# Optimization experiments

Measured on AMD Instinct MI355X. Metric: run time of the kernel, lower is better.

The kernel has to match this reference:

```python
import jax, jax.numpy as jnp
import numpy as np

B, F, V, DW, H, K, T = 32, 2048, 12000, 300, 512, 3, 32
START_ID, END_ID = 1, 2
NEG = -1e9


def lstm(x, h, c, Wx, Wh, b):
    # BasicLSTMCell with forget_bias=1.0
    z = x @ Wx + h @ Wh + b  # [N, 4H]
    i, f, g, o = jnp.split(z, 4, axis=-1)
    c2 = jax.nn.sigmoid(f + 1.0) * c + jax.nn.sigmoid(i) * jnp.tanh(g)
    h2 = jax.nn.sigmoid(o) * jnp.tanh(c2)
    return h2, c2


def beam_decode(E, Wx, Wh, b, Wl, bl, img):
    Bn = img.shape[0]
    img_t = jnp.repeat(img, K, axis=0)  # tile_batch: [B*K, F]
    h = jnp.zeros((Bn * K, H), img.dtype)
    c = jnp.zeros_like(h)
    beam_lp = jnp.tile(jnp.array([0.0] + [NEG] * (K - 1), img.dtype), (Bn, 1))  # [B,K]
    prev = jnp.full((Bn, K), START_ID, jnp.int32)
    finished = jnp.zeros((Bn, K), bool)
    lengths = jnp.zeros((Bn, K), jnp.int32)
    ids = jnp.zeros((Bn, K, T), jnp.int32)
    end_row = jnp.where(jnp.arange(V) == END_ID, 0.0, NEG)  # finished beams only emit END

    def step(carry, t):
        h, c, beam_lp, prev, finished, lengths, ids = carry
        x = jnp.concatenate([E[prev.reshape(-1)], img_t], axis=-1)  # [B*K, DW+F]
        h2, c2 = lstm(x, h, c, Wx, Wh, b)
        lp = jax.nn.log_softmax(h2 @ Wl + bl).reshape(Bn, K, V)
        lp = jnp.where(finished[:, :, None], end_row, lp)
        total = (beam_lp[:, :, None] + lp).reshape(Bn, K * V)
        scores, idx = jax.lax.top_k(total, K)  # [B,K]
        parent = idx // V
        word = (idx % V).astype(jnp.int32)
        g2 = lambda a: jnp.take_along_axis(a, parent, axis=1)
        g3 = lambda a: jnp.take_along_axis(a, parent[:, :, None], axis=1)
        h2 = g3(h2.reshape(Bn, K, H)).reshape(Bn * K, H)
        c2 = g3(c2.reshape(Bn, K, H)).reshape(Bn * K, H)
        ids = g3(ids).at[:, :, t].set(word)  # reorder hypotheses, append word
        fin_p = g2(finished)
        len_p = g2(lengths)
        lengths = jnp.where(fin_p, len_p, len_p + 1)
        finished = fin_p | (word == END_ID)
        return (h2, c2, scores, word, finished, lengths, ids), None

    carry, _ = jax.lax.scan(step, (h, c, beam_lp, prev, finished, lengths, ids), jnp.arange(T))
    return carry[6], carry[5]  # ids [B,K,T], lengths [B,K]


def teacher_rnn(E, Wx, Wh, b, img_t, seq_inputs, lengths):
    # dynamic_rnn semantics: zero outputs and frozen state past sequence_length
    N, L = seq_inputs.shape
    emb = E[seq_inputs]  # [N, L, DW]
    h0 = jnp.zeros((N, H), E.dtype)
    c0 = jnp.zeros_like(h0)

    def step(carry, xs):
        h, c = carry
        x_t, t = xs
        xin = jnp.concatenate([x_t, img_t], axis=-1)
        h2, c2 = lstm(xin, h, c, Wx, Wh, b)
        active = (t < lengths)[:, None]
        h = jnp.where(active, h2, h)
        c = jnp.where(active, c2, c)
        return (h, c), jnp.where(active, h2, 0.0)

    _, outs = jax.lax.scan(step, (h0, c0), (emb.transpose(1, 0, 2), jnp.arange(L)))
    return outs.transpose(1, 0, 2)  # [N, L, H]


def setup_inputs() -> dict:
    key = jax.random.key(0)
    ks = jax.random.split(key, 6)
    return {
        "mean_image_features": jax.random.normal(ks[0], (B, F), jnp.float32),
        "embeddings": jax.random.normal(ks[1], (V, DW), jnp.float32) * 0.1,
        "Wx": jax.random.normal(ks[2], (DW + F, 4 * H), jnp.float32) / np.sqrt(DW + F),
        "Wh": jax.random.normal(ks[3], (H, 4 * H), jnp.float32) / np.sqrt(H),
        "b_lstm": jnp.zeros((4 * H,), jnp.float32),
        "W_logits": jax.random.normal(ks[4], (H, V), jnp.float32) / np.sqrt(H),
        "b_logits": jnp.zeros((V,), jnp.float32),
    }


def reference(mean_image_features, embeddings, Wx, Wh, b_lstm, W_logits, b_logits):
    Bn = mean_image_features.shape[0]
    ids, lengths = beam_decode(embeddings, Wx, Wh, b_lstm, W_logits, b_logits, mean_image_features)
    seq_inputs = jnp.concatenate(
        [jnp.full((Bn, K, 1), START_ID, jnp.int32), ids], axis=2
    ).reshape(Bn * K, T + 1)
    img_t = jnp.repeat(mean_image_features, K, axis=0)
    acts = teacher_rnn(embeddings, Wx, Wh, b_lstm, img_t, seq_inputs, lengths.reshape(-1))
    logits = (acts @ W_logits + b_logits).reshape(Bn, K, T + 1, V)
    return logits, jnp.argmax(logits, axis=-1).astype(jnp.int32)
```

## Files before the change

### kernel.cpp

```cpp
#include <hip/hip_runtime.h>
#include <hip/hip_bf16.h>
#include <math.h>

#define NB   32
#define FDIM 2048
#define VV   12000
#define DWW  300
#define HH   512
#define KW   3
#define TDEC 32
#define SEQ  33
#define NK   96
#define G4   2048
#define START_ID 1
#define END_ID   2
#define NROWS 3168
#define NLB   188
#define INTMX 0x7fffffff
#define FLOORF (-3.0e38f)

typedef float f4v __attribute__((ext_vector_type(4)));
__device__ __forceinline__ void nt_store4(float* p, float4 v){
  f4v t; t.x=v.x; t.y=v.y; t.z=v.z; t.w=v.w;
  __builtin_nontemporal_store(t, (f4v*)p);
}

__device__ __forceinline__ float sigf(float x){ return 1.0f/(1.0f+expf(-x)); }

__device__ __forceinline__ unsigned short f2b(float x){
  __hip_bfloat16 b = __float2bfloat16(x);
  return *reinterpret_cast<unsigned short*>(&b);
}

__device__ __forceinline__ void ins3(float v, int i, float tv[3], int ti[3]){
  if (v > tv[0] || (v == tv[0] && i < ti[0])){
    tv[2]=tv[1]; ti[2]=ti[1]; tv[1]=tv[0]; ti[1]=ti[0]; tv[0]=v; ti[0]=i;
  } else if (v > tv[1] || (v == tv[1] && i < ti[1])){
    tv[2]=tv[1]; ti[2]=ti[1]; tv[1]=v; ti[1]=i;
  } else if (v > tv[2] || (v == tv[2] && i < ti[2])){
    tv[2]=v; ti[2]=i;
  }
}

__device__ __forceinline__ void flag_arrive(int* cnt){
  __hip_atomic_fetch_add(cnt, 1, __ATOMIC_RELEASE, __HIP_MEMORY_SCOPE_AGENT);
}
__device__ __forceinline__ void flag_wait(int* cnt, int target){
  while (__hip_atomic_load(cnt, __ATOMIC_ACQUIRE, __HIP_MEMORY_SCOPE_AGENT) < target)
    __builtin_amdgcn_s_sleep(1);
}

struct SArgs {
  const float *E, *Wx, *Wh, *Wl, *blog;
  float *P, *c2, *h2s, *zp, *partA, *beam_lp, *rowamax;
  int *prev, *finished, *lengths, *parst;
  int *cnt0, *cnt1;
  void *Lst;
};

__global__ __launch_bounds__(128) void k_pimg(const float* __restrict__ img,
                                              const float* __restrict__ Wx,
                                              float* __restrict__ parts)
{
  int colb = blockIdx.x, fb = blockIdx.y, tid = threadIdx.x;
  int col = colb*128 + tid;
  int f0 = fb*128;
  __shared__ float s_img[32][128];
  for (int r=0;r<32;r++) s_img[r][tid] = img[r*FDIM + f0 + tid];
  __syncthreads();
  float acc[32];
  #pragma unroll
  for (int r=0;r<32;r++) acc[r]=0.f;
  for (int f2=0; f2<128; ++f2){
    float w = Wx[(size_t)(DWW + f0 + f2)*G4 + col];
    #pragma unroll
    for (int r=0;r<32;r++) acc[r] += w * s_img[r][f2];
  }
  #pragma unroll
  for (int r=0;r<32;r++) parts[(size_t)fb*(32*G4) + r*G4 + col] = acc[r];
}

__global__ __launch_bounds__(512) void k_prep(const float* __restrict__ parts,
    const float* __restrict__ bls, const float* __restrict__ blog,
    float* __restrict__ P, float* __restrict__ beam_lp, int* __restrict__ prev,
    int* __restrict__ finished, int* __restrict__ lengths, int* __restrict__ cnts,
    float* __restrict__ bamax)
{
  int bid = blockIdx.x, tid = threadIdx.x;
  int gid = bid*512 + tid;
  float s = bls[gid & (G4-1)];
  for (int fb=0; fb<16; ++fb) s += parts[(size_t)fb*(32*G4) + gid];
  P[gid] = s;
  if (bid==0 && tid<NK){
    beam_lp[tid] = (tid%KW==0)?0.f:-1e9f;
    prev[tid]=START_ID; finished[tid]=0; lengths[tid]=0;
  }
  if (bid==1 && tid<2*TDEC) cnts[tid]=0;
  if (bid==2){
    __shared__ float s_rf[8]; __shared__ int s_ri[8];
    float bv=FLOORF; int bi=INTMX;
    for (int i=tid;i<VV;i+=512){
      float v=blog[i];
      if (v>bv || (v==bv && i<bi)){ bv=v; bi=i; }
    }
    #pragma unroll
    for (int d=1;d<64;d<<=1){
      float ov=__shfl_xor(bv,d); int oi=__shfl_xor(bi,d);
      if (ov>bv || (ov==bv && oi<bi)){ bv=ov; bi=oi; }
    }
    if ((tid&63)==0){ s_rf[tid>>6]=bv; s_ri[tid>>6]=bi; }
    __syncthreads();
    if (tid==0){
      for (int w=1;w<8;w++)
        if (s_rf[w]>bv || (s_rf[w]==bv && s_ri[w]<bi)){ bv=s_rf[w]; bi=s_ri[w]; }
      bamax[0] = (float)bi;
    }
  }
}

__global__ __launch_bounds__(512) void k_step1(SArgs a, int t)
{
  int bid = blockIdx.x, tid = threadIdx.x;
  __shared__ float smem[96*17 + 16*64];
  __shared__ int sprev[NK], spar[NK];
  if (t>0 && tid<NK){ sprev[tid]=a.prev[tid]; spar[tid]=a.parst[(t-1)*NK+tid]; }
  __syncthreads();

  {
    int colblk = bid & 31, p = bid >> 5;
    int col0 = colblk*64;
    int ks = p*104, ke = ks+104; if (ke>812) ke=812;
    float* sA = smem;
    float* sB = smem + 96*17;
    int tx = tid&15, ty = tid>>4;
    float4 acc[3];
    #pragma unroll
    for (int r=0;r<3;r++) acc[r]=make_float4(0.f,0.f,0.f,0.f);
    for (int k0=ks;k0<ke;k0+=16){
      int bk = ke-k0; if (bk>16) bk=16;
      for (int i=tid;i<96*16;i+=512){
        int n=i>>4, kk=i&15;
        float v=0.f;
        if (kk<bk){
          int kg=k0+kk;
          if (kg<DWW){
            int w = (t==0)?START_ID:sprev[n];
            v = a.E[(size_t)w*DWW+kg];
          } else if (t>0){
            v = a.h2s[((size_t)(t-1)*NK + spar[n])*HH + (kg-DWW)];
          }
        }
        sA[n*17+kk]=v;
      }
      for (int i=tid;i<16*64;i+=512){
        int kk=i>>6, cc=i&63;
        float v=0.f;
        if (kk<bk){
          int kg=k0+kk;
          v = (kg<DWW) ? a.Wx[(size_t)kg*G4+col0+cc] : a.Wh[(size_t)(kg-DWW)*G4+col0+cc];
        }
        sB[i]=v;
      }
      __syncthreads();
      #pragma unroll
      for (int kk=0;kk<16;++kk){
        float4 b4 = *(const float4*)&sB[kk*64+tx*4];
        #pragma unroll
        for (int rr=0;rr<3;rr++){
          float av = sA[(ty+rr*32)*17+kk];
          acc[rr].x += av*b4.x; acc[rr].y += av*b4.y;
          acc[rr].z += av*b4.z; acc[rr].w += av*b4.w;
        }
      }
      __syncthreads();
    }
    float* zpp = a.zp + (size_t)p*NK*G4;
    #pragma unroll
    for (int rr=0;rr<3;rr++)
      *(float4*)&zpp[(size_t)(ty+rr*32)*G4 + col0 + tx*4] = acc[rr];
  }
  __syncthreads();
  if (tid==0) flag_arrive(&a.cnt0[t]);
  if (bid >= NK) return;

  if (tid==0) flag_wait(&a.cnt0[t], 256);
  __syncthreads();
  {
    int n = bid, m = tid, bb = n/KW;
    const float* Pr = a.P + (size_t)bb*G4;
    float zi=Pr[m], zf=Pr[HH+m], zg=Pr[2*HH+m], zo=Pr[3*HH+m];
    for (int p=0;p<8;p++){
      const float* zz = a.zp + (size_t)p*NK*G4 + (size_t)n*G4;
      zi+=zz[m]; zf+=zz[HH+m]; zg+=zz[2*HH+m]; zo+=zz[3*HH+m];
    }
    float cold = (t==0) ? 0.f : a.c2[(size_t)((t-1)&1)*NK*HH + (size_t)spar[n]*HH + m];
    float c2v = sigf(zf+1.0f)*cold + sigf(zi)*tanhf(zg);
    float h2v = sigf(zo)*tanhf(c2v);
    a.c2[(size_t)(t&1)*NK*HH + (size_t)n*HH + m] = c2v;
    a.h2s[((size_t)t*NK+n)*HH + m] = h2v;
  }
}

template<int BF>
__global__ __launch_bounds__(512) void k_step2(SArgs a, int t)
{
  int bid = blockIdx.x, tid = threadIdx.x;
  __shared__ float smem[96*36 + 32*64];
  __shared__ float s_lse[KW], s_tv3[KW*3];
  __shared__ int   s_ti3[KW*3];

  {
    int col0 = bid*64;
    float* sA = smem;
    float* sB = smem + 96*36;
    int tx=tid&15, ty=tid>>4;
    float4 acc[3];
    #pragma unroll
    for (int r=0;r<3;r++) acc[r]=make_float4(0.f,0.f,0.f,0.f);
    for (int k0=0;k0<HH;k0+=32){
      for (int i=tid;i<768;i+=512){
        int row=i>>3, kq=(i&7)*4;
        *(float4*)&sA[row*36+kq] = *(const float4*)&a.h2s[((size_t)t*NK+row)*HH + k0+kq];
      }
      {
        int kk=tid>>4, c4=(tid&15)*4;
        int col=col0+c4;
        float4 v = make_float4(0.f,0.f,0.f,0.f);
        if (col < VV) v = *(const float4*)&a.Wl[(size_t)(k0+kk)*VV+col];
        *(float4*)&sB[kk*64+c4]=v;
      }
      __syncthreads();
      #pragma unroll
      for (int kk=0;kk<32;++kk){
        float4 b4 = *(const float4*)&sB[kk*64+tx*4];
        #pragma unroll
        for (int rr=0;rr<3;rr++){
          float av = sA[(ty+rr*32)*36+kk];
          acc[rr].x += av*b4.x; acc[rr].y += av*b4.y;
          acc[rr].z += av*b4.z; acc[rr].w += av*b4.w;
        }
      }
      __syncthreads();
    }
    int colg = col0 + tx*4;
    bool cval = colg < VV;
    float4 bias = make_float4(0.f,0.f,0.f,0.f);
    if (cval) bias = *(const float4*)&a.blog[colg];
    #pragma unroll
    for (int rr=0;rr<3;rr++){
      int row = ty + rr*32;
      float v0,v1,v2,v3;
      if (cval){
        v0=acc[rr].x+bias.x; v1=acc[rr].y+bias.y;
        v2=acc[rr].z+bias.z; v3=acc[rr].w+bias.w;
        size_t off = (size_t)(t*NK+row)*VV + colg;
        if (BF){
          ushort4 u;
          u.x=f2b(v0); u.y=f2b(v1); u.z=f2b(v2); u.w=f2b(v3);
          *(ushort4*)((unsigned short*)a.Lst + off) = u;
        } else {
          *(float4*)((float*)a.Lst + off) = make_float4(v0,v1,v2,v3);
        }
      } else { v0=v1=v2=v3=-INFINITY; }
      float m = fmaxf(fmaxf(v0,v1),fmaxf(v2,v3));
      #pragma unroll
      for (int d=1;d<16;d<<=1) m = fmaxf(m,__shfl_xor(m,d));
      float tv[3]={-INFINITY,-INFINITY,-INFINITY};
      int   ti[3]={INTMX,INTMX,INTMX};
      float s=0.f;
      if (cval){
        ins3(v0,colg,tv,ti); ins3(v1,colg+1,tv,ti);
        ins3(v2,colg+2,tv,ti); ins3(v3,colg+3,tv,ti);
        s = expf(v0-m)+expf(v1-m)+expf(v2-m)+expf(v3-m);
      }
      #pragma unroll
      for (int d=1;d<16;d<<=1){
        s += __shfl_xor(s,d);
        float p0=__shfl_xor(tv[0],d),p1=__shfl_xor(tv[1],d),p2=__shfl_xor(tv[2],d);
        int q0=__shfl_xor(ti[0],d),q1=__shfl_xor(ti[1],d),q2=__shfl_xor(ti[2],d);
        ins3(p0,q0,tv,ti); ins3(p1,q1,tv,ti); ins3(p2,q2,tv,ti);
      }
      if (tx==0){
        float* rp = a.partA + ((size_t)row*NLB + bid)*8;
        *(float4*)rp = make_float4(m,s,tv[0],tv[1]);
        *((float4*)rp+1) = make_float4(tv[2],__int_as_float(ti[0]),__int_as_float(ti[1]),__int_as_float(ti[2]));
      }
    }
  }
  __syncthreads();
  if (tid==0) flag_arrive(&a.cnt1[t]);
  if (bid >= NB) return;

  if (tid==0) flag_wait(&a.cnt1[t], NLB);
  __syncthreads();
  {
    int b = bid;
    int wv = tid>>6, lane = tid&63;
    if (wv < KW){
      int n = b*KW+wv;
      float M=FLOORF, S=0.f;
      float tv[3]={FLOORF,FLOORF,FLOORF}; int ti[3]={INTMX,INTMX,INTMX};
      for (int i=lane;i<NLB;i+=64){
        const float* rp = a.partA + ((size_t)n*NLB+i)*8;
        float4 r0=*(const float4*)rp, r1=*((const float4*)rp+1);
        float nm = fmaxf(M,r0.x);
        S = S*expf(M-nm) + r0.y*expf(r0.x-nm);
        M = nm;
        ins3(r0.z,__float_as_int(r1.y),tv,ti);
        ins3(r0.w,__float_as_int(r1.z),tv,ti);
        ins3(r1.x,__float_as_int(r1.w),tv,ti);
      }
      #pragma unroll
      for (int d=1;d<64;d<<=1){
        float Mo=__shfl_xor(M,d), So=__shfl_xor(S,d);
        float nm=fmaxf(M,Mo);
        S = S*expf(M-nm)+So*expf(Mo-nm);
        M=nm;
        float p0=__shfl_xor(tv[0],d),p1=__shfl_xor(tv[1],d),p2=__shfl_xor(tv[2],d);
        int q0=__shfl_xor(ti[0],d),q1=__shfl_xor(ti[1],d),q2=__shfl_xor(ti[2],d);
        ins3(p0,q0,tv,ti); ins3(p1,q1,tv,ti); ins3(p2,q2,tv,ti);
      }
      if (lane==0){
        s_lse[wv] = M + logf(S);
        #pragma unroll
        for (int j=0;j<3;j++){ s_tv3[wv*3+j]=tv[j]; s_ti3[wv*3+j]=ti[j]; }
        a.rowamax[t*NK+n] = (float)ti[0];
      }
    }
    __syncthreads();
    if (tid==0){
      float cv[3]={FLOORF,FLOORF,FLOORF}; int cf[3]={INTMX,INTMX,INTMX};
      for (int k=0;k<KW;k++){
        int n=b*KW+k;
        if (a.finished[n]){
          ins3(a.beam_lp[n], k*VV+END_ID, cv,cf);
        } else {
          float blp=a.beam_lp[n], lse=s_lse[k];
          for (int j=0;j<3;j++)
            ins3(blp + (s_tv3[k*3+j]-lse), k*VV+s_ti3[k*3+j], cv,cf);
        }
      }
      int fin_old[KW], len_old[KW];
      for (int j=0;j<KW;j++){ fin_old[j]=a.finished[b*KW+j]; len_old[j]=a.lengths[b*KW+j]; }
      for (int kp=0;kp<KW;kp++){
        int par=cf[kp]/VV, word=cf[kp]-par*VV;
        a.beam_lp[b*KW+kp]=cv[kp];
        a.prev[b*KW+kp]=word;
        a.parst[t*NK + b*KW+kp] = b*KW+par;
        int fp=fin_old[par];
        a.lengths[b*KW+kp] = fp?len_old[par]:(len_old[par]+1);
        a.finished[b*KW+kp] = fp | (word==END_ID);
      }
    }
  }
}

__global__ __launch_bounds__(128) void k_backtrack(const int* __restrict__ parst,
                                                   const int* __restrict__ lengths,
                                                   int* __restrict__ rowsrc)
{
  int n = threadIdx.x;
  if (n >= NK) return;
  int b = n / KW;
  int len = lengths[n];
  rowsrc[n*SEQ + TDEC] = -1;
  int a = n;
  for (int tau = TDEC-1; tau >= 1; --tau){
    int p = parst[tau*NK + a];
    rowsrc[n*SEQ + tau] = (tau < len) ? (tau*NK + p) : -1;
    a = p;
  }
  rowsrc[n*SEQ + 0] = b*KW;
}

template<int BF>
__global__ __launch_bounds__(512) void k_gather(const void* __restrict__ Lst,
    const int* __restrict__ rowsrc, const float* __restrict__ rowamax,
    const float* __restrict__ bamax, const float* __restrict__ blog,
    float* __restrict__ out)
{
  int row = blockIdx.x, tid = threadIdx.x;
  int src = rowsrc[row];
  float* orow = out + (size_t)row*VV;
  if (src >= 0){
    if (BF){
      const unsigned short* L = (const unsigned short*)Lst + (size_t)src*VV;
      for (int j=tid;j<VV/4;j+=512){
        ushort4 u = *(const ushort4*)&L[j*4];
        float4 v;
        v.x = __uint_as_float(((unsigned)u.x)<<16);
        v.y = __uint_as_float(((unsigned)u.y)<<16);
        v.z = __uint_as_float(((unsigned)u.z)<<16);
        v.w = __uint_as_float(((unsigned)u.w)<<16);
        nt_store4(&orow[j*4], v);
      }
    } else {
      const float* L = (const float*)Lst + (size_t)src*VV;
      for (int j=tid;j<VV/4;j+=512){
        float4 v = *(const float4*)&L[j*4];
        nt_store4(&orow[j*4], v);
      }
    }
    if (tid==0) out[(size_t)NROWS*VV + row] = rowamax[src];
  } else {
    for (int j=tid;j<VV/4;j+=512){
      float4 v = *(const float4*)&blog[j*4];
      nt_store4(&orow[j*4], v);
    }
    if (tid==0) out[(size_t)NROWS*VV + row] = bamax[0];
  }
}

extern "C" void kernel_launch(void* const* d_in, const int* in_sizes, int n_in,
                              void* d_out, int out_size, void* d_ws, size_t ws_size,
                              hipStream_t stream) {
  (void)in_sizes; (void)n_in; (void)out_size;
  const float* img  = (const float*)d_in[0];
  const float* E    = (const float*)d_in[1];
  const float* Wx   = (const float*)d_in[2];
  const float* Wh   = (const float*)d_in[3];
  const float* bls  = (const float*)d_in[4];
  const float* Wl   = (const float*)d_in[5];
  const float* blog = (const float*)d_in[6];
  float* out = (float*)d_out;

  float* ws = (float*)d_ws;
  size_t o = 0;
  float* P       = ws+o; o += (size_t)NB*G4;
  float* c2      = ws+o; o += (size_t)2*NK*HH;
  float* h2s     = ws+o; o += (size_t)TDEC*NK*HH;
  float* zp      = ws+o; o += (size_t)8*NK*G4;
  float* partA   = ws+o; o += (size_t)NK*NLB*8;
  float* beam_lp = ws+o; o += 128;
  float* rowamax = ws+o; o += (size_t)TDEC*NK;
  float* bamax   = ws+o; o += 4;
  int* prev      = (int*)(ws+o); o += 128;
  int* finished  = (int*)(ws+o); o += 128;
  int* lengths   = (int*)(ws+o); o += 128;
  int* parst     = (int*)(ws+o); o += (size_t)TDEC*NK;
  int* rowsrc    = (int*)(ws+o); o += 3328;
  int* cnts      = (int*)(ws+o); o += 64;
  o = (o+3) & ~(size_t)3;
  void* Lst      = (void*)(ws+o);

  bool f32 = (ws_size/4 > o) && ((ws_size/4 - o) >= (size_t)TDEC*NK*VV);

  SArgs a;
  a.E=E; a.Wx=Wx; a.Wh=Wh; a.Wl=Wl; a.blog=blog;
  a.P=P; a.c2=c2; a.h2s=h2s; a.zp=zp; a.partA=partA;
  a.beam_lp=beam_lp; a.rowamax=rowamax;
  a.prev=prev; a.finished=finished; a.lengths=lengths; a.parst=parst;
  a.cnt0=cnts; a.cnt1=cnts+TDEC;
  a.Lst=Lst;

  k_pimg<<<dim3(16,16),128,0,stream>>>(img, Wx, zp);
  k_prep<<<128,512,0,stream>>>(zp, bls, blog, P, beam_lp, prev, finished, lengths, cnts, bamax);

  if (f32){
    for (int t=0;t<TDEC;t++){
      k_step1<<<256,512,0,stream>>>(a,t);
      k_step2<0><<<NLB,512,0,stream>>>(a,t);
    }
    k_backtrack<<<1,128,0,stream>>>(parst, lengths, rowsrc);
    k_gather<0><<<NROWS,512,0,stream>>>(Lst,rowsrc,rowamax,bamax,blog,out);
  } else {
    for (int t=0;t<TDEC;t++){
      k_step1<<<256,512,0,stream>>>(a,t);
      k_step2<1><<<NLB,512,0,stream>>>(a,t);
    }
    k_backtrack<<<1,128,0,stream>>>(parst, lengths, rowsrc);
    k_gather<1><<<NROWS,512,0,stream>>>(Lst,rowsrc,rowamax,bamax,blog,out);
  }
}
```

Before: 3.069 ms.

## Fuse per-step decode kernels into one persistent cooperative kernel with flag barriers

Replaces the 64 per-timestep launches (step1/step2) plus the backtrack kernel with a single cooperatively launched persistent kernel of 256 blocks. The stages within each step are ordered by atomic-counter flag barriers, with an end-of-step barrier over the beam-update blocks. This removes kernel launch gaps and lets blocks run ahead between stages, at the cost of spin-waiting and one grid-wide wait per step. It also switches the fp32 logits stores to nontemporal stores.

```diff
diff --git a/kernel.cpp b/kernel.cpp
--- a/kernel.cpp
+++ b/kernel.cpp
@@ -16,6 +16,8 @@
 #define END_ID   2
 #define NROWS 3168
 #define NLB   188
+#define GRID  256
+#define BLK   512
 #define INTMX 0x7fffffff
 #define FLOORF (-3.0e38f)
 
@@ -42,19 +44,22 @@
   }
 }
 
-__device__ __forceinline__ void flag_arrive(int* cnt){
+__device__ __forceinline__ void bar_arrive(int* cnt){
   __hip_atomic_fetch_add(cnt, 1, __ATOMIC_RELEASE, __HIP_MEMORY_SCOPE_AGENT);
 }
-__device__ __forceinline__ void flag_wait(int* cnt, int target){
-  while (__hip_atomic_load(cnt, __ATOMIC_ACQUIRE, __HIP_MEMORY_SCOPE_AGENT) < target)
-    __builtin_amdgcn_s_sleep(1);
-}
-
-struct SArgs {
+__device__ __forceinline__ void bar_wait(int* cnt, int target){
+  if (threadIdx.x==0){
+    while (__hip_atomic_load(cnt, __ATOMIC_ACQUIRE, __HIP_MEMORY_SCOPE_AGENT) < target)
+      __builtin_amdgcn_s_sleep(1);
+  }
+  __syncthreads();
+}
+
+struct PArgs {
   const float *E, *Wx, *Wh, *Wl, *blog;
   float *P, *c2, *h2s, *zp, *partA, *beam_lp, *rowamax;
-  int *prev, *finished, *lengths, *parst;
-  int *cnt0, *cnt1;
+  int *prev, *finished, *lengths, *parst, *rowsrc;
+  int *fZ, *fG, *fL, *fS;
   void *Lst;
 };
 
@@ -95,7 +100,7 @@
     beam_lp[tid] = (tid%KW==0)?0.f:-1e9f;
     prev[tid]=START_ID; finished[tid]=0; lengths[tid]=0;
   }
-  if (bid==1 && tid<2*TDEC) cnts[tid]=0;
+  if (bid==1 && tid<4*TDEC) cnts[tid]=0;
   if (bid==2){
     __shared__ float s_rf[8]; __shared__ int s_ri[8];
     float bv=FLOORF; int bi=INTMX;
@@ -118,259 +123,253 @@
   }
 }
 
-__global__ __launch_bounds__(512) void k_step1(SArgs a, int t)
-{
-  int bid = blockIdx.x, tid = threadIdx.x;
-  __shared__ float smem[96*17 + 16*64];
-  __shared__ int sprev[NK], spar[NK];
-  if (t>0 && tid<NK){ sprev[tid]=a.prev[tid]; spar[tid]=a.parst[(t-1)*NK+tid]; }
-  __syncthreads();
-
-  {
-    int colblk = bid & 31, p = bid >> 5;
-    int col0 = colblk*64;
-    int ks = p*104, ke = ks+104; if (ke>812) ke=812;
-    float* sA = smem;
-    float* sB = smem + 96*17;
-    int tx = tid&15, ty = tid>>4;
-    float4 acc[3];
-    #pragma unroll
-    for (int r=0;r<3;r++) acc[r]=make_float4(0.f,0.f,0.f,0.f);
-    for (int k0=ks;k0<ke;k0+=16){
-      int bk = ke-k0; if (bk>16) bk=16;
-      for (int i=tid;i<96*16;i+=512){
-        int n=i>>4, kk=i&15;
-        float v=0.f;
-        if (kk<bk){
-          int kg=k0+kk;
-          if (kg<DWW){
-            int w = (t==0)?START_ID:sprev[n];
-            v = a.E[(size_t)w*DWW+kg];
-          } else if (t>0){
-            v = a.h2s[((size_t)(t-1)*NK + spar[n])*HH + (kg-DWW)];
-          }
-        }
-        sA[n*17+kk]=v;
-      }
-      for (int i=tid;i<16*64;i+=512){
-        int kk=i>>6, cc=i&63;
-        float v=0.f;
-        if (kk<bk){
-          int kg=k0+kk;
-          v = (kg<DWW) ? a.Wx[(size_t)kg*G4+col0+cc] : a.Wh[(size_t)(kg-DWW)*G4+col0+cc];
-        }
-        sB[i]=v;
-      }
-      __syncthreads();
-      #pragma unroll
-      for (int kk=0;kk<16;++kk){
-        float4 b4 = *(const float4*)&sB[kk*64+tx*4];
-        #pragma unroll
-        for (int rr=0;rr<3;rr++){
-          float av = sA[(ty+rr*32)*17+kk];
-          acc[rr].x += av*b4.x; acc[rr].y += av*b4.y;
-          acc[rr].z += av*b4.z; acc[rr].w += av*b4.w;
-        }
-      }
-      __syncthreads();
-    }
-    float* zpp = a.zp + (size_t)p*NK*G4;
-    #pragma unroll
-    for (int rr=0;rr<3;rr++)
-      *(float4*)&zpp[(size_t)(ty+rr*32)*G4 + col0 + tx*4] = acc[rr];
-  }
-  __syncthreads();
-  if (tid==0) flag_arrive(&a.cnt0[t]);
-  if (bid >= NK) return;
-
-  if (tid==0) flag_wait(&a.cnt0[t], 256);
-  __syncthreads();
-  {
-    int n = bid, m = tid, bb = n/KW;
-    const float* Pr = a.P + (size_t)bb*G4;
-    float zi=Pr[m], zf=Pr[HH+m], zg=Pr[2*HH+m], zo=Pr[3*HH+m];
-    for (int p=0;p<8;p++){
-      const float* zz = a.zp + (size_t)p*NK*G4 + (size_t)n*G4;
-      zi+=zz[m]; zf+=zz[HH+m]; zg+=zz[2*HH+m]; zo+=zz[3*HH+m];
-    }
-    float cold = (t==0) ? 0.f : a.c2[(size_t)((t-1)&1)*NK*HH + (size_t)spar[n]*HH + m];
-    float c2v = sigf(zf+1.0f)*cold + sigf(zi)*tanhf(zg);
-    float h2v = sigf(zo)*tanhf(c2v);
-    a.c2[(size_t)(t&1)*NK*HH + (size_t)n*HH + m] = c2v;
-    a.h2s[((size_t)t*NK+n)*HH + m] = h2v;
-  }
-}
-
 template<int BF>
-__global__ __launch_bounds__(512) void k_step2(SArgs a, int t)
+__global__ __launch_bounds__(BLK) void k_persist(PArgs a)
 {
   int bid = blockIdx.x, tid = threadIdx.x;
   __shared__ float smem[96*36 + 32*64];
+  __shared__ int sprev[NK], spar[NK];
   __shared__ float s_lse[KW], s_tv3[KW*3];
   __shared__ int   s_ti3[KW*3];
 
-  {
-    int col0 = bid*64;
-    float* sA = smem;
-    float* sB = smem + 96*36;
-    int tx=tid&15, ty=tid>>4;
-    float4 acc[3];
-    #pragma unroll
-    for (int r=0;r<3;r++) acc[r]=make_float4(0.f,0.f,0.f,0.f);
-    for (int k0=0;k0<HH;k0+=32){
-      for (int i=tid;i<768;i+=512){
-        int row=i>>3, kq=(i&7)*4;
-        *(float4*)&sA[row*36+kq] = *(const float4*)&a.h2s[((size_t)t*NK+row)*HH + k0+kq];
-      }
-      {
-        int kk=tid>>4, c4=(tid&15)*4;
-        int col=col0+c4;
-        float4 v = make_float4(0.f,0.f,0.f,0.f);
-        if (col < VV) v = *(const float4*)&a.Wl[(size_t)(k0+kk)*VV+col];
-        *(float4*)&sB[kk*64+c4]=v;
-      }
+  for (int t=0;t<TDEC;++t){
+    if (tid<NK){ sprev[tid]=a.prev[tid]; if (t>0) spar[tid]=a.parst[(t-1)*NK+tid]; }
+    __syncthreads();
+
+    {
+      int colblk = bid & 31, p = bid >> 5;
+      int col0 = colblk*64;
+      int ks = p*104, ke = ks+104; if (ke>812) ke=812;
+      float* sA = smem;
+      float* sB = smem + 96*17;
+      int tx = tid&15, ty = tid>>4;
+      float4 acc[3];
+      #pragma unroll
+      for (int r=0;r<3;r++) acc[r]=make_float4(0.f,0.f,0.f,0.f);
+      for (int k0=ks;k0<ke;k0+=16){
+        int bk = ke-k0; if (bk>16) bk=16;
+        for (int i=tid;i<96*16;i+=BLK){
+          int n=i>>4, kk=i&15;
+          float v=0.f;
+          if (kk<bk){
+            int kg=k0+kk;
+            if (kg<DWW){
+              int w = (t==0)?START_ID:sprev[n];
+              v = a.E[(size_t)w*DWW+kg];
+            } else if (t>0){
+              v = a.h2s[((size_t)(t-1)*NK + spar[n])*HH + (kg-DWW)];
+            }
+          }
+          sA[n*17+kk]=v;
+        }
+        for (int i=tid;i<16*64;i+=BLK){
+          int kk=i>>6, cc=i&63;
+          float v=0.f;
+          if (kk<bk){
+            int kg=k0+kk;
+            v = (kg<DWW) ? a.Wx[(size_t)kg*G4+col0+cc] : a.Wh[(size_t)(kg-DWW)*G4+col0+cc];
+          }
+          sB[i]=v;
+        }
+        __syncthreads();
+        #pragma unroll
+        for (int kk=0;kk<16;++kk){
+          float4 b4 = *(const float4*)&sB[kk*64+tx*4];
+          #pragma unroll
+          for (int rr=0;rr<3;rr++){
+            float av = sA[(ty+rr*32)*17+kk];
+            acc[rr].x += av*b4.x; acc[rr].y += av*b4.y;
+            acc[rr].z += av*b4.z; acc[rr].w += av*b4.w;
+          }
+        }
+        __syncthreads();
+      }
+      float* zpp = a.zp + (size_t)p*NK*G4;
+      #pragma unroll
+      for (int rr=0;rr<3;rr++)
+        *(float4*)&zpp[(size_t)(ty+rr*32)*G4 + col0 + tx*4] = acc[rr];
+    }
+    __syncthreads();
+    if (tid==0) bar_arrive(&a.fZ[t]);
+
+    if (bid < NK){
+      bar_wait(&a.fZ[t], GRID);
+      int n = bid, m = tid, bb = n/KW;
+      const float* Pr = a.P + (size_t)bb*G4;
+      float zi=Pr[m], zf=Pr[HH+m], zg=Pr[2*HH+m], zo=Pr[3*HH+m];
+      for (int p=0;p<8;p++){
+        const float* zz = a.zp + (size_t)p*NK*G4 + (size_t)n*G4;
+        zi+=zz[m]; zf+=zz[HH+m]; zg+=zz[2*HH+m]; zo+=zz[3*HH+m];
+      }
+      float cold = (t==0) ? 0.f : a.c2[(size_t)((t-1)&1)*NK*HH + (size_t)spar[n]*HH + m];
+      float c2v = sigf(zf+1.0f)*cold + sigf(zi)*tanhf(zg);
+      float h2v = sigf(zo)*tanhf(c2v);
+      a.c2[(size_t)(t&1)*NK*HH + (size_t)n*HH + m] = c2v;
+      a.h2s[((size_t)t*NK+n)*HH + m] = h2v;
       __syncthreads();
+      if (tid==0) bar_arrive(&a.fG[t]);
+    }
+
+    if (bid < NLB){
+      bar_wait(&a.fG[t], NK);
+      int col0 = bid*64;
+      float* sA = smem;
+      float* sB = smem + 96*36;
+      int tx=tid&15, ty=tid>>4;
+      float4 acc[3];
       #pragma unroll
-      for (int kk=0;kk<32;++kk){
-        float4 b4 = *(const float4*)&sB[kk*64+tx*4];
+      for (int r=0;r<3;r++) acc[r]=make_float4(0.f,0.f,0.f,0.f);
+      for (int k0=0;k0<HH;k0+=32){
+        for (int i=tid;i<768;i+=BLK){
+          int row=i>>3, kq=(i&7)*4;
+          *(float4*)&sA[row*36+kq] = *(const float4*)&a.h2s[((size_t)t*NK+row)*HH + k0+kq];
+        }
+        {
+          int kk=tid>>4, c4=(tid&15)*4;
+          int col=col0+c4;
+          float4 v = make_float4(0.f,0.f,0.f,0.f);
+          if (col < VV) v = *(const float4*)&a.Wl[(size_t)(k0+kk)*VV+col];
+          *(float4*)&sB[kk*64+c4]=v;
+        }
+        __syncthreads();
         #pragma unroll
-        for (int rr=0;rr<3;rr++){
-          float av = sA[(ty+rr*32)*36+kk];
-          acc[rr].x += av*b4.x; acc[rr].y += av*b4.y;
-          acc[rr].z += av*b4.z; acc[rr].w += av*b4.w;
+        for (int kk=0;kk<32;++kk){
+          float4 b4 = *(const float4*)&sB[kk*64+tx*4];
+          #pragma unroll
+          for (int rr=0;rr<3;rr++){
+            float av = sA[(ty+rr*32)*36+kk];
+            acc[rr].x += av*b4.x; acc[rr].y += av*b4.y;
+            acc[rr].z += av*b4.z; acc[rr].w += av*b4.w;
+          }
+        }
+        __syncthreads();
+      }
+      int colg = col0 + tx*4;
+      bool cval = colg < VV;
+      float4 bias = make_float4(0.f,0.f,0.f,0.f);
+      if (cval) bias = *(const float4*)&a.blog[colg];
+      #pragma unroll
+      for (int rr=0;rr<3;rr++){
+        int row = ty + rr*32;
+        float v0,v1,v2,v3;
+        if (cval){
+          v0=acc[rr].x+bias.x; v1=acc[rr].y+bias.y;
+          v2=acc[rr].z+bias.z; v3=acc[rr].w+bias.w;
+          size_t off = (size_t)(t*NK+row)*VV + colg;
+          if (BF){
+            ushort4 u;
+            u.x=f2b(v0); u.y=f2b(v1); u.z=f2b(v2); u.w=f2b(v3);
+            *(ushort4*)((unsigned short*)a.Lst + off) = u;
+          } else {
+            nt_store4((float*)a.Lst + off, make_float4(v0,v1,v2,v3));
+          }
+        } else { v0=v1=v2=v3=-INFINITY; }
+        float m = fmaxf(fmaxf(v0,v1),fmaxf(v2,v3));
+        #pragma unroll
+        for (int d=1;d<16;d<<=1) m = fmaxf(m,__shfl_xor(m,d));
+        float tv[3]={-INFINITY,-INFINITY,-INFINITY};
+        int   ti[3]={INTMX,INTMX,INTMX};
+        float s=0.f;
+        if (cval){
+          ins3(v0,colg,tv,ti); ins3(v1,colg+1,tv,ti);
+          ins3(v2,colg+2,tv,ti); ins3(v3,colg+3,tv,ti);
+          s = expf(v0-m)+expf(v1-m)+expf(v2-m)+expf(v3-m);
+        }
+        #pragma unroll
+        for (int d=1;d<16;d<<=1){
+          s += __shfl_xor(s,d);
+          float p0=__shfl_xor(tv[0],d),p1=__shfl_xor(tv[1],d),p2=__shfl_xor(tv[2],d);
+          int q0=__shfl_xor(ti[0],d),q1=__shfl_xor(ti[1],d),q2=__shfl_xor(ti[2],d);
+          ins3(p0,q0,tv,ti); ins3(p1,q1,tv,ti); ins3(p2,q2,tv,ti);
+        }
+        if (tx==0){
+          float* rp = a.partA + ((size_t)row*NLB + bid)*8;
+          *(float4*)rp = make_float4(m,s,tv[0],tv[1]);
+          *((float4*)rp+1) = make_float4(tv[2],__int_as_float(ti[0]),__int_as_float(ti[1]),__int_as_float(ti[2]));
         }
       }
       __syncthreads();
-    }
-    int colg = col0 + tx*4;
-    bool cval = colg < VV;
-    float4 bias = make_float4(0.f,0.f,0.f,0.f);
-    if (cval) bias = *(const float4*)&a.blog[colg];
-    #pragma unroll
-    for (int rr=0;rr<3;rr++){
-      int row = ty + rr*32;
-      float v0,v1,v2,v3;
-      if (cval){
-        v0=acc[rr].x+bias.x; v1=acc[rr].y+bias.y;
-        v2=acc[rr].z+bias.z; v3=acc[rr].w+bias.w;
-        size_t off = (size_t)(t*NK+row)*VV + colg;
-        if (BF){
-          ushort4 u;
-          u.x=f2b(v0); u.y=f2b(v1); u.z=f2b(v2); u.w=f2b(v3);
-          *(ushort4*)((unsigned short*)a.Lst + off) = u;
-        } else {
-          *(float4*)((float*)a.Lst + off) = make_float4(v0,v1,v2,v3);
-        }
-      } else { v0=v1=v2=v3=-INFINITY; }
-      float m = fmaxf(fmaxf(v0,v1),fmaxf(v2,v3));
-      #pragma unroll
-      for (int d=1;d<16;d<<=1) m = fmaxf(m,__shfl_xor(m,d));
-      float tv[3]={-INFINITY,-INFINITY,-INFINITY};
-      int   ti[3]={INTMX,INTMX,INTMX};
-      float s=0.f;
-      if (cval){
-        ins3(v0,colg,tv,ti); ins3(v1,colg+1,tv,ti);
-        ins3(v2,colg+2,tv,ti); ins3(v3,colg+3,tv,ti);
-        s = expf(v0-m)+expf(v1-m)+expf(v2-m)+expf(v3-m);
-      }
-      #pragma unroll
-      for (int d=1;d<16;d<<=1){
-        s += __shfl_xor(s,d);
-        float p0=__shfl_xor(tv[0],d),p1=__shfl_xor(tv[1],d),p2=__shfl_xor(tv[2],d);
-        int q0=__shfl_xor(ti[0],d),q1=__shfl_xor(ti[1],d),q2=__shfl_xor(ti[2],d);
-        ins3(p0,q0,tv,ti); ins3(p1,q1,tv,ti); ins3(p2,q2,tv,ti);
-      }
-      if (tx==0){
-        float* rp = a.partA + ((size_t)row*NLB + bid)*8;
-        *(float4*)rp = make_float4(m,s,tv[0],tv[1]);
-        *((float4*)rp+1) = make_float4(tv[2],__int_as_float(ti[0]),__int_as_float(ti[1]),__int_as_float(ti[2]));
-      }
-    }
-  }
-  __syncthreads();
-  if (tid==0) flag_arrive(&a.cnt1[t]);
-  if (bid >= NB) return;
-
-  if (tid==0) flag_wait(&a.cnt1[t], NLB);
-  __syncthreads();
-  {
-    int b = bid;
-    int wv = tid>>6, lane = tid&63;
-    if (wv < KW){
-      int n = b*KW+wv;
-      float M=FLOORF, S=0.f;
-      float tv[3]={FLOORF,FLOORF,FLOORF}; int ti[3]={INTMX,INTMX,INTMX};
-      for (int i=lane;i<NLB;i+=64){
-        const float* rp = a.partA + ((size_t)n*NLB+i)*8;
-        float4 r0=*(const float4*)rp, r1=*((const float4*)rp+1);
-        float nm = fmaxf(M,r0.x);
-        S = S*expf(M-nm) + r0.y*expf(r0.x-nm);
-        M = nm;
-        ins3(r0.z,__float_as_int(r1.y),tv,ti);
-        ins3(r0.w,__float_as_int(r1.z),tv,ti);
-        ins3(r1.x,__float_as_int(r1.w),tv,ti);
-      }
-      #pragma unroll
-      for (int d=1;d<64;d<<=1){
-        float Mo=__shfl_xor(M,d), So=__shfl_xor(S,d);
-        float nm=fmaxf(M,Mo);
-        S = S*expf(M-nm)+So*expf(Mo-nm);
-        M=nm;
-        float p0=__shfl_xor(tv[0],d),p1=__shfl_xor(tv[1],d),p2=__shfl_xor(tv[2],d);
-        int q0=__shfl_xor(ti[0],d),q1=__shfl_xor(ti[1],d),q2=__shfl_xor(ti[2],d);
-        ins3(p0,q0,tv,ti); ins3(p1,q1,tv,ti); ins3(p2,q2,tv,ti);
-      }
-      if (lane==0){
-        s_lse[wv] = M + logf(S);
+      if (tid==0) bar_arrive(&a.fL[t]);
+    }
+
+    if (bid < NB){
+      bar_wait(&a.fL[t], NLB);
+      int b = bid;
+      int wv = tid>>6, lane = tid&63;
+      if (wv < KW){
+        int n = b*KW+wv;
+        float M=FLOORF, S=0.f;
+        float tv[3]={FLOORF,FLOORF,FLOORF}; int ti[3]={INTMX,INTMX,INTMX};
+        for (int i=lane;i<NLB;i+=64){
+          const float* rp = a.partA + ((size_t)n*NLB+i)*8;
+          float4 r0=*(const float4*)rp, r1=*((const float4*)rp+1);
+          float nm = fmaxf(M,r0.x);
+          S = S*expf(M-nm) + r0.y*expf(r0.x-nm);
+          M = nm;
+          ins3(r0.z,__float_as_int(r1.y),tv,ti);
+          ins3(r0.w,__float_as_int(r1.z),tv,ti);
+          ins3(r1.x,__float_as_int(r1.w),tv,ti);
+        }
         #pragma unroll
-        for (int j=0;j<3;j++){ s_tv3[wv*3+j]=tv[j]; s_ti3[wv*3+j]=ti[j]; }
-        a.rowamax[t*NK+n] = (float)ti[0];
-      }
-    }
-    __syncthreads();
-    if (tid==0){
-      float cv[3]={FLOORF,FLOORF,FLOORF}; int cf[3]={INTMX,INTMX,INTMX};
-      for (int k=0;k<KW;k++){
-        int n=b*KW+k;
-        if (a.finished[n]){
-          ins3(a.beam_lp[n], k*VV+END_ID, cv,cf);
-        } else {
-          float blp=a.beam_lp[n], lse=s_lse[k];
-          for (int j=0;j<3;j++)
-            ins3(blp + (s_tv3[k*3+j]-lse), k*VV+s_ti3[k*3+j], cv,cf);
-        }
-      }
-      int fin_old[KW], len_old[KW];
-      for (int j=0;j<KW;j++){ fin_old[j]=a.finished[b*KW+j]; len_old[j]=a.lengths[b*KW+j]; }
-      for (int kp=0;kp<KW;kp++){
-        int par=cf[kp]/VV, word=cf[kp]-par*VV;
-        a.beam_lp[b*KW+kp]=cv[kp];
-        a.prev[b*KW+kp]=word;
-        a.parst[t*NK + b*KW+kp] = b*KW+par;
-        int fp=fin_old[par];
-        a.lengths[b*KW+kp] = fp?len_old[par]:(len_old[par]+1);
-        a.finished[b*KW+kp] = fp | (word==END_ID);
-      }
-    }
-  }
-}
-
-__global__ __launch_bounds__(128) void k_backtrack(const int* __restrict__ parst,
-                                                   const int* __restrict__ lengths,
-                                                   int* __restrict__ rowsrc)
-{
-  int n = threadIdx.x;
-  if (n >= NK) return;
-  int b = n / KW;
-  int len = lengths[n];
-  rowsrc[n*SEQ + TDEC] = -1;
-  int a = n;
-  for (int tau = TDEC-1; tau >= 1; --tau){
-    int p = parst[tau*NK + a];
-    rowsrc[n*SEQ + tau] = (tau < len) ? (tau*NK + p) : -1;
-    a = p;
-  }
-  rowsrc[n*SEQ + 0] = b*KW;
+        for (int d=1;d<64;d<<=1){
+          float Mo=__shfl_xor(M,d), So=__shfl_xor(S,d);
+          float nm=fmaxf(M,Mo);
+          S = S*expf(M-nm)+So*expf(Mo-nm);
+          M=nm;
+          float p0=__shfl_xor(tv[0],d),p1=__shfl_xor(tv[1],d),p2=__shfl_xor(tv[2],d);
+          int q0=__shfl_xor(ti[0],d),q1=__shfl_xor(ti[1],d),q2=__shfl_xor(ti[2],d);
+          ins3(p0,q0,tv,ti); ins3(p1,q1,tv,ti); ins3(p2,q2,tv,ti);
+        }
+        if (lane==0){
+          s_lse[wv] = M + logf(S);
+          #pragma unroll
+          for (int j=0;j<3;j++){ s_tv3[wv*3+j]=tv[j]; s_ti3[wv*3+j]=ti[j]; }
+          a.rowamax[t*NK+n] = (float)ti[0];
+        }
+      }
+      __syncthreads();
+      if (tid==0){
+        float cv[3]={FLOORF,FLOORF,FLOORF}; int cf[3]={INTMX,INTMX,INTMX};
+        for (int k=0;k<KW;k++){
+          int n=b*KW+k;
+          if (a.finished[n]){
+            ins3(a.beam_lp[n], k*VV+END_ID, cv,cf);
+          } else {
+            float blp=a.beam_lp[n], lse=s_lse[k];
+            for (int j=0;j<3;j++)
+              ins3(blp + (s_tv3[k*3+j]-lse), k*VV+s_ti3[k*3+j], cv,cf);
+          }
+        }
+        int fin_old[KW], len_old[KW];
+        for (int j=0;j<KW;j++){ fin_old[j]=a.finished[b*KW+j]; len_old[j]=a.lengths[b*KW+j]; }
+        for (int kp=0;kp<KW;kp++){
+          int par=cf[kp]/VV, word=cf[kp]-par*VV;
+          a.beam_lp[b*KW+kp]=cv[kp];
+          a.prev[b*KW+kp]=word;
+          a.parst[t*NK + b*KW+kp] = b*KW+par;
+          int fp=fin_old[par];
+          a.lengths[b*KW+kp] = fp?len_old[par]:(len_old[par]+1);
+          a.finished[b*KW+kp] = fp | (word==END_ID);
+        }
+        bar_arrive(&a.fS[t]);
+      }
+    }
+
+    bar_wait(&a.fS[t], NB);
+  }
+
+  if (bid==0 && tid<NK){
+    int n=tid, b=n/KW;
+    int len = a.lengths[n];
+    a.rowsrc[n*SEQ+TDEC] = -1;
+    int cur=n;
+    for (int tau=TDEC-1; tau>=1; --tau){
+      int p = a.parst[tau*NK+cur];
+      a.rowsrc[n*SEQ+tau] = (tau<len)? (tau*NK+p) : -1;
+      cur=p;
+    }
+    a.rowsrc[n*SEQ+0] = b*KW;
+  }
 }
 
 template<int BF>
@@ -439,36 +438,29 @@
   int* lengths   = (int*)(ws+o); o += 128;
   int* parst     = (int*)(ws+o); o += (size_t)TDEC*NK;
   int* rowsrc    = (int*)(ws+o); o += 3328;
-  int* cnts      = (int*)(ws+o); o += 64;
+  int* cnts      = (int*)(ws+o); o += 256;
   o = (o+3) & ~(size_t)3;
   void* Lst      = (void*)(ws+o);
 
   bool f32 = (ws_size/4 > o) && ((ws_size/4 - o) >= (size_t)TDEC*NK*VV);
 
-  SArgs a;
+  PArgs a;
   a.E=E; a.Wx=Wx; a.Wh=Wh; a.Wl=Wl; a.blog=blog;
   a.P=P; a.c2=c2; a.h2s=h2s; a.zp=zp; a.partA=partA;
   a.beam_lp=beam_lp; a.rowamax=rowamax;
-  a.prev=prev; a.finished=finished; a.lengths=lengths; a.parst=parst;
-  a.cnt0=cnts; a.cnt1=cnts+TDEC;
+  a.prev=prev; a.finished=finished; a.lengths=lengths; a.parst=parst; a.rowsrc=rowsrc;
+  a.fZ=cnts; a.fG=cnts+TDEC; a.fL=cnts+2*TDEC; a.fS=cnts+3*TDEC;
   a.Lst=Lst;
+  void* kp[] = { (void*)&a };
 
   k_pimg<<<dim3(16,16),128,0,stream>>>(img, Wx, zp);
   k_prep<<<128,512,0,stream>>>(zp, bls, blog, P, beam_lp, prev, finished, lengths, cnts, bamax);
 
   if (f32){
-    for (int t=0;t<TDEC;t++){
-      k_step1<<<256,512,0,stream>>>(a,t);
-      k_step2<0><<<NLB,512,0,stream>>>(a,t);
-    }
-    k_backtrack<<<1,128,0,stream>>>(parst, lengths, rowsrc);
+    hipLaunchCooperativeKernel(k_persist<0>, dim3(GRID), dim3(BLK), kp, 0u, stream);
     k_gather<0><<<NROWS,512,0,stream>>>(Lst,rowsrc,rowamax,bamax,blog,out);
   } else {
-    for (int t=0;t<TDEC;t++){
-      k_step1<<<256,512,0,stream>>>(a,t);
-      k_step2<1><<<NLB,512,0,stream>>>(a,t);
-    }
-    k_backtrack<<<1,128,0,stream>>>(parst, lengths, rowsrc);
+    hipLaunchCooperativeKernel(k_persist<1>, dim3(GRID), dim3(BLK), kp, 0u, stream);
     k_gather<1><<<NROWS,512,0,stream>>>(Lst,rowsrc,rowamax,bamax,blog,out);
   }
 }
```

Result: slower. 4.902 ms (+59.7%).
